# Kernel optimization log

Hardware: AMD Instinct MI355X
Metric: run time of the kernel (lower is better)

The kernel has to match this reference:

```python
import jax, jax.numpy as jnp
import numpy as np

B, S, D = 2, 2048, 4096
N_HEADS, N_KV_HEADS = 32, 8
HEAD_DIM = D // N_HEADS  # 128
N_REP = N_HEADS // N_KV_HEADS
NEG_INF = -1e9  # finite stand-in for -inf additive causal mask


def apply_rotary_emb(x, freqs_cis):
    # x: [b, s, h, hd]; freqs_cis: [s, hd//2, 2] (cos, sin)
    b, s, h, hd = x.shape
    xr = x.reshape(b, s, h, hd // 2, 2)
    fc = freqs_cis.reshape(1, s, 1, hd // 2, 2)
    o0 = xr[..., 0] * fc[..., 0] - xr[..., 1] * fc[..., 1]
    o1 = xr[..., 1] * fc[..., 0] + xr[..., 0] * fc[..., 1]
    return jnp.stack([o0, o1], axis=-1).reshape(b, s, h, hd)


def setup_inputs() -> dict:
    key = jax.random.key(0)
    ks = jax.random.split(key, 6)
    x = jax.random.normal(ks[0], (B, S, D), dtype=jnp.float32)
    # weights stored torch-style: [out_features, in_features]
    wq = jax.random.normal(ks[1], (N_HEADS * HEAD_DIM, D), dtype=jnp.float32) * 0.02
    wk = jax.random.normal(ks[2], (N_KV_HEADS * HEAD_DIM, D), dtype=jnp.float32) * 0.02
    wv = jax.random.normal(ks[3], (N_KV_HEADS * HEAD_DIM, D), dtype=jnp.float32) * 0.02
    wo = jax.random.normal(ks[4], (D, N_HEADS * HEAD_DIM), dtype=jnp.float32) * 0.02
    # rotary table (Llama-style, theta=10000)
    inv_freq = 1.0 / (10000.0 ** (np.arange(0, HEAD_DIM, 2, dtype=np.float32) / HEAD_DIM))
    angles = np.arange(S, dtype=np.float32)[:, None] * inv_freq[None, :]
    freqs_cis = jnp.asarray(np.stack([np.cos(angles), np.sin(angles)], axis=-1))  # [S, hd//2, 2]
    # additive causal mask
    mask = jnp.where(jnp.tril(jnp.ones((S, S), dtype=bool)), 0.0, NEG_INF).astype(jnp.float32)
    return {"x": x, "start_pos": 0, "freqs_cis": freqs_cis, "mask": mask,
            "wq": wq, "wk": wk, "wv": wv, "wo": wo}


def reference(x, start_pos, freqs_cis, mask, wq, wk, wv, wo):
    b, s, _ = x.shape
    xq = jnp.einsum('bsd,ed->bse', x, wq).reshape(b, s, N_HEADS, HEAD_DIM)
    xk = jnp.einsum('bsd,ed->bse', x, wk).reshape(b, s, N_KV_HEADS, HEAD_DIM)
    xv = jnp.einsum('bsd,ed->bse', x, wv).reshape(b, s, N_KV_HEADS, HEAD_DIM)
    xq = apply_rotary_emb(xq, freqs_cis)
    xk = apply_rotary_emb(xk, freqs_cis)
    # repeat_kv (repeat_interleave along head dim)
    xk = jnp.repeat(xk, N_REP, axis=2)
    xv = jnp.repeat(xv, N_REP, axis=2)
    q = xq.transpose(0, 2, 1, 3)  # [b, h, s, hd]
    k = xk.transpose(0, 2, 1, 3)
    v = xv.transpose(0, 2, 1, 3)
    scores = jnp.einsum('bhqd,bhkd->bhqk', q, k) / jnp.sqrt(jnp.float32(HEAD_DIM))
    scores = scores + mask[None, None, :, :]
    probs = jax.nn.softmax(scores.astype(jnp.float32), axis=-1).astype(q.dtype)
    out = jnp.einsum('bhqk,bhkd->bhqd', probs, v)
    out = out.transpose(0, 2, 1, 3).reshape(b, s, N_HEADS * HEAD_DIM)
    return jnp.einsum('bse,de->bsd', out, wo)
```

## Files before the change

### kernel.cpp

```cpp
#include <hip/hip_runtime.h>
#include <cstdint>
#include <cstddef>

#define B_   2
#define S_   2048
#define D_   4096
#define H_   32
#define KVH_ 8
#define HD_  128

typedef unsigned short u16;
typedef short     bf16x8 __attribute__((ext_vector_type(8)));
typedef float     f32x4  __attribute__((ext_vector_type(4)));
typedef float     f32x16 __attribute__((ext_vector_type(16)));
typedef u16       u16x8  __attribute__((ext_vector_type(8)));
typedef uint32_t  u32x2  __attribute__((ext_vector_type(2)));
typedef uint32_t  u32x4  __attribute__((ext_vector_type(4)));

__device__ __forceinline__ u16 f2bf(float f) {
  union { float f; uint32_t u; } v; v.f = f;
  uint32_t u = v.u;
  return (u16)((u + 0x7fffu + ((u >> 16) & 1u)) >> 16);
}
__device__ __forceinline__ float bf2f(u16 h) {
  union { uint32_t u; float f; } v; v.u = ((uint32_t)h) << 16;
  return v.f;
}
__device__ __forceinline__ uint32_t cvtpk(float lo, float hi_) {
  uint32_t r; asm("v_cvt_pk_bf16_f32 %0, %1, %2" : "=v"(r) : "v"(lo), "v"(hi_)); return r;
}
__device__ __forceinline__ float exp2v(float x) {
  float r; asm("v_exp_f32 %0, %1" : "=v"(r) : "v"(x)); return r;
}

__device__ __forceinline__ void gl_lds16(const void* g, void* l) {
  __builtin_amdgcn_global_load_lds(
      (const __attribute__((address_space(1))) void*)g,
      (__attribute__((address_space(3))) void*)l, 16, 0, 0);
}

#define MFMA(a, b, c)  __builtin_amdgcn_mfma_f32_16x16x32_bf16((a), (b), (c), 0, 0, 0)
#define MFMA32(a, b, c) __builtin_amdgcn_mfma_f32_32x32x16_bf16((a), (b), (c), 0, 0, 0)
#define PLSWAP(x, y) asm volatile("v_permlane32_swap_b32 %0, %1" : "+v"(x), "+v"(y))

__global__ void cast_kernel(const float* __restrict__ in, u16* __restrict__ out, int n8) {
  int i = blockIdx.x * blockDim.x + threadIdx.x;
  if (i >= n8) return;
  const float4* p = (const float4*)in + (size_t)i * 2;
  float4 a = p[0], b = p[1];
  u16x8 r;
  r[0] = f2bf(a.x); r[1] = f2bf(a.y); r[2] = f2bf(a.z); r[3] = f2bf(a.w);
  r[4] = f2bf(b.x); r[5] = f2bf(b.y); r[6] = f2bf(b.z); r[7] = f2bf(b.w);
  *((u16x8*)out + i) = r;
}

template <bool OUT_F32>
__global__ __launch_bounds__(256, 2)
void gemm_bt(const u16* __restrict__ A, const u16* __restrict__ Bw,
             void* __restrict__ C, int M, int N, int K) {
  __shared__ u16 lA[128 * 32];
  __shared__ u16 lB[128 * 32];
  const int tid = threadIdx.x;
  const int w = tid >> 6, l = tid & 63;
  const int lc = l & 15, lg = l >> 4;
  const int bn = blockIdx.x, bm = blockIdx.y;
  const int wr = w >> 1, wc = w & 1;
  const u16* Ab = A + (size_t)(bm * 128) * K;
  const u16* Bb = Bw + (size_t)(bn * 128) * K;
  const int srow = l >> 2;
  const int scol = (l & 3) * 8;

  f32x4 acc[4][4];
#pragma unroll
  for (int i = 0; i < 4; ++i)
#pragma unroll
    for (int j = 0; j < 4; ++j) acc[i][j] = (f32x4){0.f, 0.f, 0.f, 0.f};

  const int nk = K >> 5;
  for (int kt = 0; kt < nk; ++kt) {
    const int k0 = kt * 32;
    __syncthreads();
#pragma unroll
    for (int i = 0; i < 2; ++i) {
      const int rowA = (w * 2 + i) * 16;
      gl_lds16(Ab + (size_t)(rowA + srow) * K + k0 + scol, &lA[rowA * 32]);
      gl_lds16(Bb + (size_t)(rowA + srow) * K + k0 + scol, &lB[rowA * 32]);
    }
    __syncthreads();
    bf16x8 af[4], bfr[4];
#pragma unroll
    for (int mi = 0; mi < 4; ++mi)
      af[mi] = *(const bf16x8*)&lA[(wr * 64 + mi * 16 + lc) * 32 + lg * 8];
#pragma unroll
    for (int ni = 0; ni < 4; ++ni)
      bfr[ni] = *(const bf16x8*)&lB[(wc * 64 + ni * 16 + lc) * 32 + lg * 8];
#pragma unroll
    for (int mi = 0; mi < 4; ++mi)
#pragma unroll
      for (int ni = 0; ni < 4; ++ni)
        acc[mi][ni] = MFMA(af[mi], bfr[ni], acc[mi][ni]);
  }

#pragma unroll
  for (int mi = 0; mi < 4; ++mi)
#pragma unroll
    for (int ni = 0; ni < 4; ++ni)
#pragma unroll
      for (int r = 0; r < 4; ++r) {
        const int row = bm * 128 + wr * 64 + mi * 16 + lg * 4 + r;
        const int col = bn * 128 + wc * 64 + ni * 16 + lc;
        if constexpr (OUT_F32)
          ((float*)C)[(size_t)row * N + col] = acc[mi][ni][r];
        else
          ((u16*)C)[(size_t)row * N + col] = f2bf(acc[mi][ni][r]);
      }
}

template <bool OUT_F32>
__global__ __launch_bounds__(512, 2)
void gemm256_bt(const u16* __restrict__ A, const u16* __restrict__ Bw,
                void* __restrict__ C, int M, int N, int K) {
  __shared__ u16 sA[2 * 256 * 64];
  __shared__ u16 sB[2 * 256 * 64];
  const int tid = threadIdx.x;
  const int w = tid >> 6, l = tid & 63;
  const int lc = l & 15, lg = l >> 4;
  const int wm = w >> 2, wn = w & 3;
  const int nbn = N >> 8;
  const int nwg = (M >> 8) * nbn;
  const int cpx = nwg >> 3;
  const int lin = blockIdx.x;
  const int swz = (lin & 7) * cpx + (lin >> 3);
  const int bm = swz / nbn, bn = swz % nbn;
  const u16* Ab = A + (size_t)(bm * 256) * K;
  const u16* Bb = Bw + (size_t)(bn * 256) * K;
  const int lr = l >> 3;
  const int scc = ((l & 7) ^ lr) * 8;
  int cxg[2];
#pragma unroll
  for (int kk = 0; kk < 2; ++kk) cxg[kk] = ((kk * 4 + lg) ^ (lc & 7)) * 8;

  f32x4 acc[8][4];
#pragma unroll
  for (int i = 0; i < 8; ++i)
#pragma unroll
    for (int j = 0; j < 4; ++j) acc[i][j] = (f32x4){0.f, 0.f, 0.f, 0.f};

  auto STAGEA = [&](int buf, int t1, int h) {
    const int k0 = t1 * 64;
#pragma unroll
    for (int j = 0; j < 2; ++j) {
      const int r0 = h * 128 + w * 16 + j * 8;
      gl_lds16(Ab + (size_t)(r0 + lr) * K + k0 + scc, &sA[buf * 16384 + r0 * 64]);
    }
  };
  auto STAGEB = [&](int buf, int t1, int h) {
    const int k0 = t1 * 64;
#pragma unroll
    for (int j = 0; j < 2; ++j) {
      const int r0 = h * 128 + w * 16 + j * 8;
      gl_lds16(Bb + (size_t)(r0 + lr) * K + k0 + scc, &sB[buf * 16384 + r0 * 64]);
    }
  };

  bf16x8 afr[4][2], b0r[2][2], b1r[2][2];
  auto LDA = [&](int base, int ha) {
#pragma unroll
    for (int mi = 0; mi < 4; ++mi)
#pragma unroll
      for (int kk = 0; kk < 2; ++kk)
        afr[mi][kk] = *(const bf16x8*)
            &sA[base + (ha * 128 + wm * 64 + mi * 16 + lc) * 64 + cxg[kk]];
  };
  auto LDB0 = [&](int base) {
#pragma unroll
    for (int ni = 0; ni < 2; ++ni)
#pragma unroll
      for (int kk = 0; kk < 2; ++kk)
        b0r[ni][kk] = *(const bf16x8*)
            &sB[base + (wn * 32 + ni * 16 + lc) * 64 + cxg[kk]];
  };
  auto LDB1 = [&](int base) {
#pragma unroll
    for (int ni = 0; ni < 2; ++ni)
#pragma unroll
      for (int kk = 0; kk < 2; ++kk)
        b1r[ni][kk] = *(const bf16x8*)
            &sB[base + (128 + wn * 32 + ni * 16 + lc) * 64 + cxg[kk]];
  };

#define VMW(N_) asm volatile("s_waitcnt vmcnt(" #N_ ")" ::: "memory")
#define BARR do { __builtin_amdgcn_s_barrier(); asm volatile("" ::: "memory"); } while (0)
#define LGKM do { asm volatile("s_waitcnt lgkmcnt(0)" ::: "memory"); \
                  __builtin_amdgcn_sched_barrier(0); } while (0)
#define MMQ(HA, HB, BF) do { __builtin_amdgcn_s_setprio(1); \
  _Pragma("unroll") for (int kk = 0; kk < 2; ++kk) \
  _Pragma("unroll") for (int mi = 0; mi < 4; ++mi) \
  _Pragma("unroll") for (int ni = 0; ni < 2; ++ni) \
    acc[(HA) * 4 + mi][(HB) * 2 + ni] = \
        MFMA(afr[mi][kk], BF[ni][kk], acc[(HA) * 4 + mi][(HB) * 2 + ni]); \
  __builtin_amdgcn_s_setprio(0); } while (0)

  const int nk = K >> 6;
  STAGEA(0, 0, 0); STAGEB(0, 0, 0);
  STAGEB(0, 0, 1); STAGEA(0, 0, 1);
  STAGEA(1, 1, 0); STAGEB(1, 1, 0);
  VMW(8);
  BARR;
  LDA(0, 0); LDB0(0);

  for (int t = 0; t < nk; ++t) {
    const int cur = t & 1;
    const int cb = cur * 16384;
    const int nbb = (cur ^ 1) * 16384;
    const bool n1 = (t + 1 < nk), n2 = (t + 2 < nk);

    if (n1) VMW(6); else VMW(2);
    BARR;
    if (n1) { STAGEB(cur ^ 1, t + 1, 1); STAGEA(cur ^ 1, t + 1, 1); }
    LGKM;
    MMQ(0, 0, b0r);
    LDB1(cb);

    if (n1) VMW(8); else VMW(0);
    BARR;
    LGKM;
    MMQ(0, 1, b1r);
    LDA(cb, 1);

    BARR;
    if (n2) STAGEA(cur, t + 2, 0);
    LGKM;
    MMQ(1, 1, b1r);

    if (n1) { if (n2) VMW(6); else VMW(4); }
    BARR;
    if (n2) STAGEB(cur, t + 2, 0);
    LGKM;
    MMQ(1, 0, b0r);
    if (n1) { LDA(nbb, 0); LDB0(nbb); }
  }
#undef VMW
#undef BARR
#undef LGKM
#undef MMQ

#pragma unroll
  for (int ha = 0; ha < 2; ++ha)
#pragma unroll
    for (int mi = 0; mi < 4; ++mi)
#pragma unroll
      for (int hb = 0; hb < 2; ++hb)
#pragma unroll
        for (int ni = 0; ni < 2; ++ni)
#pragma unroll
          for (int r = 0; r < 4; ++r) {
            const int row = bm * 256 + ha * 128 + wm * 64 + mi * 16 + lg * 4 + r;
            const int col = bn * 256 + hb * 128 + wn * 32 + ni * 16 + lc;
            if constexpr (OUT_F32)
              ((float*)C)[(size_t)row * N + col] = acc[ha * 4 + mi][hb * 2 + ni][r];
            else
              ((u16*)C)[(size_t)row * N + col] = f2bf(acc[ha * 4 + mi][hb * 2 + ni][r]);
          }
}

template <int NH, int STRIDE, int OFF>
__global__ void rope_kernel(const u16* __restrict__ lin, const float* __restrict__ fr,
                            u16* __restrict__ out, float scale) {
  int idx = blockIdx.x * 256 + threadIdx.x;
  const int total = B_ * S_ * NH * 64;
  if (idx >= total) return;
  const int i = idx & 63;
  const int h = (idx >> 6) % NH;
  const int t = idx / (64 * NH);
  const int s = t & (S_ - 1);
  const int b = t >> 11;
  const size_t src = (size_t)t * STRIDE + OFF + h * HD_ + 2 * i;
  const float x0 = bf2f(lin[src]);
  const float x1 = bf2f(lin[src + 1]);
  const float2 cs = ((const float2*)fr)[s * 64 + i];
  const float o0 = (x0 * cs.x - x1 * cs.y) * scale;
  const float o1 = (x1 * cs.x + x0 * cs.y) * scale;
  const size_t dst = ((size_t)((b * NH + h) * S_ + s)) * HD_ + 2 * i;
  out[dst] = f2bf(o0);
  out[dst + 1] = f2bf(o1);
}

__global__ void vtrans_kernel(const u16* __restrict__ kvlin, u16* __restrict__ vt) {
  __shared__ u16 tile[32][33];
  const int tx = threadIdx.x, ty = threadIdx.y;
  const int s0 = blockIdx.x * 32;
  const int d0 = blockIdx.y * 32;
  const int bk = blockIdx.z;
  const int b = bk >> 3, kv = bk & 7;
#pragma unroll
  for (int r = 0; r < 4; ++r) {
    const int s = s0 + ty + r * 8;
    tile[ty + r * 8][tx] =
        kvlin[((size_t)(b * S_ + s)) * 2048 + 1024 + kv * HD_ + d0 + tx];
  }
  __syncthreads();
#pragma unroll
  for (int r = 0; r < 4; ++r) {
    const int d = d0 + ty + r * 8;
    vt[((size_t)bk * HD_ + d) * S_ + s0 + tx] = tile[tx][ty + r * 8];
  }
}

__global__ __launch_bounds__(256, 2)
void attn_kernel(const u16* __restrict__ Q, const u16* __restrict__ K,
                 const u16* __restrict__ V, u16* __restrict__ O) {
  __shared__ u16 sK[2][64 * HD_];
  __shared__ u16 sV[2][HD_ * 64];
  const int tid = threadIdx.x;
  const int w = tid >> 6, l = tid & 63;
  const int hi = l >> 5, q32 = l & 31;
  const int kv = blockIdx.y, b = blockIdx.z;
  const int h = kv * 4 + w;
  const u16* Kp = K + ((size_t)(b * KVH_ + kv) * S_) * HD_;
  const u16* Vp = V + ((size_t)(b * KVH_ + kv) * HD_) * S_;

  int koff[4], voff[4];
#pragma unroll
  for (int i = 0; i < 4; ++i) {
    const int kr = w * 16 + i * 4 + (l >> 4);
    koff[i] = kr * HD_ + (((l & 15) ^ (kr & 7))) * 8;
    const int vr = w * 32 + i * 8 + (l >> 3);
    voff[i] = vr * S_ + (((l & 7) ^ (vr & 7))) * 8;
  }
  int cx[8];
#pragma unroll
  for (int c = 0; c < 8; ++c) cx[c] = ((c * 2 + hi) ^ (l & 7)) * 8;

  auto STAGE = [&](int bufi, int ti) {
    const u16* kg = Kp + (size_t)ti * (64 * HD_);
    const u16* vg = Vp + (size_t)ti * 64;
#pragma unroll
    for (int i = 0; i < 4; ++i) {
      gl_lds16(kg + koff[i], &sK[bufi][(w * 16 + i * 4) * HD_]);
      gl_lds16(vg + voff[i], &sV[bufi][(w * 32 + i * 8) * 64]);
    }
  };

  int cur = 0;
  for (int seg = 0; seg < 2; ++seg) {
    const int qt = seg ? (63 - blockIdx.x) : blockIdx.x;
    const int qg = qt * 32 + q32;
    const u16* Qp = Q + ((size_t)(b * H_ + h) * S_ + qt * 32) * HD_;

    bf16x8 qf[8];
#pragma unroll
    for (int ds = 0; ds < 8; ++ds)
      qf[ds] = *(const bf16x8*)(Qp + (size_t)q32 * HD_ + ds * 16 + hi * 8);
    asm volatile("s_waitcnt vmcnt(0)" ::: "memory");

    f32x16 out[4];
#pragma unroll
    for (int d = 0; d < 4; ++d)
#pragma unroll
      for (int r = 0; r < 16; ++r) out[d][r] = 0.f;
    float mrun = -1e30f, lrun = 0.f;

    const int nt = (qt >> 1) + 1;
    STAGE(cur, 0);

    for (int t = 0; t < nt; ++t) {
      if (t + 1 < nt) {
        STAGE(cur ^ 1, t + 1);
        asm volatile("s_waitcnt vmcnt(8)" ::: "memory");
      } else {
        asm volatile("s_waitcnt vmcnt(0)" ::: "memory");
      }
      __builtin_amdgcn_s_barrier();
      asm volatile("" ::: "memory");

      f32x16 sc0, sc1;
#pragma unroll
      for (int r = 0; r < 16; ++r) { sc0[r] = 0.f; sc1[r] = 0.f; }
      __builtin_amdgcn_s_setprio(1);
#pragma unroll
      for (int ds = 0; ds < 8; ++ds) {
        bf16x8 kf0 = *(const bf16x8*)&sK[cur][q32 * HD_ + cx[ds]];
        bf16x8 kf1 = *(const bf16x8*)&sK[cur][(32 + q32) * HD_ + cx[ds]];
        sc0 = MFMA32(kf0, qf[ds], sc0);
        sc1 = MFMA32(kf1, qf[ds], sc1);
      }
      __builtin_amdgcn_s_setprio(0);

      const bool diag = (t == nt - 1);
      float p0[16], p1[16];
#pragma unroll
      for (int r = 0; r < 16; ++r) {
        const int krow = (r & 3) + 8 * (r >> 2) + 4 * hi;
        float v0 = sc0[r], v1 = sc1[r];
        if (diag) {
          if (t * 64 + krow > qg) v0 = -1e9f;
          if (t * 64 + 32 + krow > qg) v1 = -1e9f;
        }
        p0[r] = v0; p1[r] = v1;
      }
      float rm = -1e30f;
#pragma unroll
      for (int r = 0; r < 16; ++r) rm = fmaxf(rm, fmaxf(p0[r], p1[r]));
      rm = fmaxf(rm, __shfl_xor(rm, 32, 64));
      if (!__all(rm <= mrun + 8.0f)) {
        const float mnew = fmaxf(mrun, rm);
        const float alpha = exp2v(mrun - mnew);
        mrun = mnew;
        lrun *= alpha;
#pragma unroll
        for (int d = 0; d < 4; ++d) out[d] *= alpha;
      }
      float sum = 0.f;
#pragma unroll
      for (int r = 0; r < 16; ++r) {
        p0[r] = exp2v(p0[r] - mrun);
        p1[r] = exp2v(p1[r] - mrun);
        sum += p0[r] + p1[r];
      }
      sum += __shfl_xor(sum, 32, 64);
      lrun += sum;
      uint32_t pk0[8], pk1[8];
#pragma unroll
      for (int g = 0; g < 4; ++g) {
        pk0[2 * g]     = cvtpk(p0[4 * g], p0[4 * g + 1]);
        pk0[2 * g + 1] = cvtpk(p0[4 * g + 2], p0[4 * g + 3]);
        pk1[2 * g]     = cvtpk(p1[4 * g], p1[4 * g + 1]);
        pk1[2 * g + 1] = cvtpk(p1[4 * g + 2], p1[4 * g + 3]);
      }
      PLSWAP(pk0[0], pk0[2]); PLSWAP(pk0[1], pk0[3]);
      PLSWAP(pk0[4], pk0[6]); PLSWAP(pk0[5], pk0[7]);
      PLSWAP(pk1[0], pk1[2]); PLSWAP(pk1[1], pk1[3]);
      PLSWAP(pk1[4], pk1[6]); PLSWAP(pk1[5], pk1[7]);
      bf16x8 pa[4];
      pa[0] = __builtin_bit_cast(bf16x8, (u32x4){pk0[0], pk0[1], pk0[2], pk0[3]});
      pa[1] = __builtin_bit_cast(bf16x8, (u32x4){pk0[4], pk0[5], pk0[6], pk0[7]});
      pa[2] = __builtin_bit_cast(bf16x8, (u32x4){pk1[0], pk1[1], pk1[2], pk1[3]});
      pa[3] = __builtin_bit_cast(bf16x8, (u32x4){pk1[4], pk1[5], pk1[6], pk1[7]});
      __builtin_amdgcn_s_setprio(1);
#pragma unroll
      for (int d = 0; d < 4; ++d) {
        const int vbase = (d * 32 + q32) * 64;
#pragma unroll
        for (int kk = 0; kk < 4; ++kk) {
          bf16x8 vf = *(const bf16x8*)&sV[cur][vbase + cx[kk]];
          out[d] = MFMA32(vf, pa[kk], out[d]);
        }
      }
      __builtin_amdgcn_s_setprio(0);
      asm volatile("" ::: "memory");
      __builtin_amdgcn_s_barrier();
      cur ^= 1;
    }

    const float inv = 1.0f / lrun;
    u16* myS = ((u16*)sK) + w * 4096;
#pragma unroll
    for (int d = 0; d < 4; ++d)
#pragma unroll
      for (int rq = 0; rq < 4; ++rq) {
        u32x2 pw;
        pw[0] = cvtpk(out[d][rq * 4 + 0] * inv, out[d][rq * 4 + 1] * inv);
        pw[1] = cvtpk(out[d][rq * 4 + 2] * inv, out[d][rq * 4 + 3] * inv);
        const int gin = (d * 8 + rq * 2 + hi) ^ (q32 & 15);
        *(u32x2*)&myS[q32 * 128 + gin * 4] = pw;
      }
    asm volatile("s_waitcnt lgkmcnt(0)" ::: "memory");
    __builtin_amdgcn_sched_barrier(0);
    const int rr = l >> 4;
    const int cc = l & 15;
#pragma unroll
    for (int p = 0; p < 8; ++p) {
      const int q = p * 4 + rr;
      const int ga = (2 * cc) ^ (q & 15);
      const int gb = (2 * cc + 1) ^ (q & 15);
      u32x2 va = *(const u32x2*)&myS[q * 128 + ga * 4];
      u32x2 vb = *(const u32x2*)&myS[q * 128 + gb * 4];
      u32x4 val = {va[0], va[1], vb[0], vb[1]};
      *(u32x4*)&O[((size_t)(b * S_ + qt * 32 + q)) * (H_ * HD_) + h * HD_ + cc * 8] = val;
    }
    if (seg == 0) {
      asm volatile("" ::: "memory");
      __builtin_amdgcn_s_barrier();
    }
  }
}

extern "C" void kernel_launch(void* const* d_in, const int* in_sizes, int n_in,
                              void* d_out, int out_size, void* d_ws, size_t ws_size,
                              hipStream_t stream) {
  const float* x     = (const float*)d_in[0];
  const float* freqs = (const float*)d_in[2];
  const float* wq    = (const float*)d_in[4];
  const float* wk    = (const float*)d_in[5];
  const float* wv    = (const float*)d_in[6];
  const float* wo    = (const float*)d_in[7];

  char* ws = (char*)d_ws;
  u16* xb    = (u16*)(ws + 0);
  u16* wqb   = (u16*)(ws + 33554432);
  u16* wkb   = (u16*)(ws + 67108864);
  u16* wvb   = (u16*)(ws + 75497472);
  u16* qlin  = (u16*)(ws + 83886080);
  u16* kvlin = (u16*)(ws + 117440512);
  u16* qr   = wqb;
  u16* kr   = wkb;
  u16* vt   = wvb;
  u16* aout = qlin;
  u16* wob  = xb;

  cast_kernel<<<8192, 256, 0, stream>>>(x, xb, 2097152);
  cast_kernel<<<8192, 256, 0, stream>>>(wq, wqb, 2097152);
  cast_kernel<<<2048, 256, 0, stream>>>(wk, wkb, 524288);
  cast_kernel<<<2048, 256, 0, stream>>>(wv, wvb, 524288);
  gemm256_bt<false><<<256, 512, 0, stream>>>(xb, wqb, qlin, 4096, 4096, 4096);
  gemm_bt<false><<<dim3(16, 32), 256, 0, stream>>>(xb, wkb, kvlin, 4096, 2048, 4096);
  rope_kernel<32, 4096, 0><<<32768, 256, 0, stream>>>(qlin, freqs, qr,
      0.08838834764831845f * 1.4426950408889634f);
  rope_kernel<8, 2048, 0><<<8192, 256, 0, stream>>>(kvlin, freqs, kr, 1.0f);
  vtrans_kernel<<<dim3(64, 4, 16), dim3(32, 8), 0, stream>>>(kvlin, vt);
  attn_kernel<<<dim3(32, 8, 2), 256, 0, stream>>>(qr, kr, vt, aout);
  cast_kernel<<<8192, 256, 0, stream>>>(wo, wob, 2097152);
  gemm256_bt<true><<<256, 512, 0, stream>>>(aout, wob, d_out, 4096, 4096, 4096);
}
```

Baseline: 546.9 us.

## Fuse Q rotary embedding into Q projection GEMM epilogue and reorder GEMM pipeline

The Q projection GEMM now applies rotary embedding and the softmax scale in its epilogue. It pairs adjacent columns with a lane shuffle and writes Q straight into the head-major layout, which removes the separate Q rope kernel and its round trip through global memory. The main loop is also reorganised: LDS fragment loads move to the start of each stage, and the wait counts and barriers change (one barrier per iteration removed). The epilogue's strided head-major stores and per-element table loads may be less coalesced, and the new pipeline order may expose more LDS latency.

```diff
diff --git a/kernel.cpp b/kernel.cpp
--- a/kernel.cpp
+++ b/kernel.cpp
@@ -116,10 +116,11 @@
       }
 }
 
-template <bool OUT_F32>
+template <int MODE>
 __global__ __launch_bounds__(512, 2)
 void gemm256_bt(const u16* __restrict__ A, const u16* __restrict__ Bw,
-                void* __restrict__ C, int M, int N, int K) {
+                void* __restrict__ C, int M, int N, int K,
+                const float* __restrict__ fr, float qscale) {
   __shared__ u16 sA[2 * 256 * 64];
   __shared__ u16 sB[2 * 256 * 64];
   const int tid = threadIdx.x;
@@ -164,29 +165,29 @@
   };
 
   bf16x8 afr[4][2], b0r[2][2], b1r[2][2];
-  auto LDA = [&](int base, int ha) {
+  auto LDA = [&](int cb, int ha) {
 #pragma unroll
     for (int mi = 0; mi < 4; ++mi)
 #pragma unroll
       for (int kk = 0; kk < 2; ++kk)
         afr[mi][kk] = *(const bf16x8*)
-            &sA[base + (ha * 128 + wm * 64 + mi * 16 + lc) * 64 + cxg[kk]];
+            &sA[cb + (ha * 128 + wm * 64 + mi * 16 + lc) * 64 + cxg[kk]];
   };
-  auto LDB0 = [&](int base) {
+  auto LDB0 = [&](int cb) {
 #pragma unroll
     for (int ni = 0; ni < 2; ++ni)
 #pragma unroll
       for (int kk = 0; kk < 2; ++kk)
         b0r[ni][kk] = *(const bf16x8*)
-            &sB[base + (wn * 32 + ni * 16 + lc) * 64 + cxg[kk]];
+            &sB[cb + (wn * 32 + ni * 16 + lc) * 64 + cxg[kk]];
   };
-  auto LDB1 = [&](int base) {
+  auto LDB1 = [&](int cb) {
 #pragma unroll
     for (int ni = 0; ni < 2; ++ni)
 #pragma unroll
       for (int kk = 0; kk < 2; ++kk)
         b1r[ni][kk] = *(const bf16x8*)
-            &sB[base + (128 + wn * 32 + ni * 16 + lc) * 64 + cxg[kk]];
+            &sB[cb + (128 + wn * 32 + ni * 16 + lc) * 64 + cxg[kk]];
   };
 
 #define VMW(N_) asm volatile("s_waitcnt vmcnt(" #N_ ")" ::: "memory")
@@ -205,40 +206,35 @@
   STAGEA(0, 0, 0); STAGEB(0, 0, 0);
   STAGEB(0, 0, 1); STAGEA(0, 0, 1);
   STAGEA(1, 1, 0); STAGEB(1, 1, 0);
-  VMW(8);
-  BARR;
-  LDA(0, 0); LDB0(0);
 
   for (int t = 0; t < nk; ++t) {
     const int cur = t & 1;
     const int cb = cur * 16384;
-    const int nbb = (cur ^ 1) * 16384;
+    const int nb = cur ^ 1;
     const bool n1 = (t + 1 < nk), n2 = (t + 2 < nk);
 
-    if (n1) VMW(6); else VMW(2);
+    VMW(8);
     BARR;
-    if (n1) { STAGEB(cur ^ 1, t + 1, 1); STAGEA(cur ^ 1, t + 1, 1); }
+    LDA(cb, 0); LDB0(cb);
+    if (n1) { STAGEB(nb, t + 1, 1); STAGEA(nb, t + 1, 1); }
     LGKM;
     MMQ(0, 0, b0r);
+
+    if (n1) VMW(10); else VMW(2);
+    BARR;
     LDB1(cb);
+    LGKM;
+    MMQ(0, 1, b1r);
 
     if (n1) VMW(8); else VMW(0);
     BARR;
-    LGKM;
-    MMQ(0, 1, b1r);
     LDA(cb, 1);
-
-    BARR;
     if (n2) STAGEA(cur, t + 2, 0);
     LGKM;
     MMQ(1, 1, b1r);
 
-    if (n1) { if (n2) VMW(6); else VMW(4); }
-    BARR;
     if (n2) STAGEB(cur, t + 2, 0);
-    LGKM;
     MMQ(1, 0, b0r);
-    if (n1) { LDA(nbb, 0); LDB0(nbb); }
   }
 #undef VMW
 #undef BARR
@@ -257,10 +253,21 @@
           for (int r = 0; r < 4; ++r) {
             const int row = bm * 256 + ha * 128 + wm * 64 + mi * 16 + lg * 4 + r;
             const int col = bn * 256 + hb * 128 + wn * 32 + ni * 16 + lc;
-            if constexpr (OUT_F32)
-              ((float*)C)[(size_t)row * N + col] = acc[ha * 4 + mi][hb * 2 + ni][r];
-            else
-              ((u16*)C)[(size_t)row * N + col] = f2bf(acc[ha * 4 + mi][hb * 2 + ni][r]);
+            const float v = acc[ha * 4 + mi][hb * 2 + ni][r];
+            if constexpr (MODE == 1) {
+              ((float*)C)[(size_t)row * N + col] = v;
+            } else if constexpr (MODE == 0) {
+              ((u16*)C)[(size_t)row * N + col] = f2bf(v);
+            } else {
+              const float pv = __shfl_xor(v, 1, 64);
+              const int b = row >> 11, s = row & (S_ - 1);
+              const int h = col >> 7, d = col & 127;
+              const float2 cs = ((const float2*)fr)[s * 64 + (d >> 1)];
+              const float o = ((lc & 1) == 0) ? (v * cs.x - pv * cs.y)
+                                              : (v * cs.x + pv * cs.y);
+              ((u16*)C)[(((size_t)(b * H_ + h) * S_ + s)) * HD_ + d] =
+                  f2bf(o * qscale);
+            }
           }
 }
 
@@ -501,25 +508,26 @@
   u16* wqb   = (u16*)(ws + 33554432);
   u16* wkb   = (u16*)(ws + 67108864);
   u16* wvb   = (u16*)(ws + 75497472);
-  u16* qlin  = (u16*)(ws + 83886080);
+  u16* qrope = (u16*)(ws + 83886080);
   u16* kvlin = (u16*)(ws + 117440512);
-  u16* qr   = wqb;
   u16* kr   = wkb;
   u16* vt   = wvb;
-  u16* aout = qlin;
+  u16* aout = wqb;
   u16* wob  = xb;
+
+  const float qscale = 0.08838834764831845f * 1.4426950408889634f;
 
   cast_kernel<<<8192, 256, 0, stream>>>(x, xb, 2097152);
   cast_kernel<<<8192, 256, 0, stream>>>(wq, wqb, 2097152);
   cast_kernel<<<2048, 256, 0, stream>>>(wk, wkb, 524288);
   cast_kernel<<<2048, 256, 0, stream>>>(wv, wvb, 524288);
-  gemm256_bt<false><<<256, 512, 0, stream>>>(xb, wqb, qlin, 4096, 4096, 4096);
+  gemm256_bt<2><<<256, 512, 0, stream>>>(xb, wqb, qrope, 4096, 4096, 4096,
+                                         freqs, qscale);
   gemm_bt<false><<<dim3(16, 32), 256, 0, stream>>>(xb, wkb, kvlin, 4096, 2048, 4096);
-  rope_kernel<32, 4096, 0><<<32768, 256, 0, stream>>>(qlin, freqs, qr,
-      0.08838834764831845f * 1.4426950408889634f);
   rope_kernel<8, 2048, 0><<<8192, 256, 0, stream>>>(kvlin, freqs, kr, 1.0f);
   vtrans_kernel<<<dim3(64, 4, 16), dim3(32, 8), 0, stream>>>(kvlin, vt);
-  attn_kernel<<<dim3(32, 8, 2), 256, 0, stream>>>(qr, kr, vt, aout);
+  attn_kernel<<<dim3(32, 8, 2), 256, 0, stream>>>(qrope, kr, vt, aout);
   cast_kernel<<<8192, 256, 0, stream>>>(wo, wob, 2097152);
-  gemm256_bt<true><<<256, 512, 0, stream>>>(aout, wob, d_out, 4096, 4096, 4096);
-}
+  gemm256_bt<1><<<256, 512, 0, stream>>>(aout, wob, d_out, 4096, 4096, 4096,
+                                         nullptr, 0.f);
+}
```

Result: faster. 497.9 us (-9.0%).
